# Kernel optimization log

Measured on AMD Instinct MI355X. Metric: run time of the kernel, lower is better.

Reference implementation:

```python
import jax, jax.numpy as jnp
import numpy as np

B, N_I, N_H1, N_H2, N_H3, N_H4 = 4096, 1024, 1024, 1024, 2048, 1024


def _linear_params(key, n_out, n_in, gain=1.0):
    kw, kb = jax.random.split(key)
    # xavier_uniform on weight, torch default uniform bias ~ U(-1/sqrt(n_in), 1/sqrt(n_in))
    limit = gain * np.sqrt(6.0 / (n_in + n_out))
    W = jax.random.uniform(kw, (n_out, n_in), jnp.float32, -limit, limit)
    bl = 1.0 / np.sqrt(n_in)
    b = jax.random.uniform(kb, (n_out,), jnp.float32, -bl, bl)
    return W, b


def setup_inputs() -> dict:
    key = jax.random.key(0)
    ks = jax.random.split(key, 16)
    inp = {
        "X": jax.random.normal(ks[0], (B, N_I), jnp.float32),
        "hidden1": jax.random.normal(ks[1], (B, N_H1), jnp.float32),
        "hidden2": jax.random.normal(ks[2], (B, N_H2), jnp.float32),
        "cell1": jax.random.normal(ks[3], (B, N_H1), jnp.float32),
        "cell2": jax.random.normal(ks[4], (B, N_H2), jnp.float32),
    }
    # LSTM1 gates: Linear(n_i + n_h1, n_h1)
    inp["Wf1"], inp["bf1"] = _linear_params(ks[5], N_H1, N_I + N_H1, 1.0)
    inp["Wi1"], inp["bi1"] = _linear_params(ks[6], N_H1, N_I + N_H1, 1.0)
    inp["Wc1"], inp["bc1"] = _linear_params(ks[7], N_H1, N_I + N_H1, 5.0 / 3.0)
    inp["Wo1"], inp["bo1"] = _linear_params(ks[8], N_H1, N_I + N_H1, 1.0)
    # LSTM2 gates: Linear(n_h1 + n_h2, n_h2)
    inp["Wf2"], inp["bf2"] = _linear_params(ks[9], N_H2, N_H1 + N_H2, 1.0)
    inp["Wi2"], inp["bi2"] = _linear_params(ks[10], N_H2, N_H1 + N_H2, 1.0)
    inp["Wc2"], inp["bc2"] = _linear_params(ks[11], N_H2, N_H1 + N_H2, 5.0 / 3.0)
    inp["Wo2"], inp["bo2"] = _linear_params(ks[12], N_H2, N_H1 + N_H2, 1.0)
    # MLP head
    inp["W3"], inp["b3"] = _linear_params(ks[13], N_H3, N_H2, np.sqrt(2.0))
    inp["W4"], inp["b4"] = _linear_params(ks[14], N_H4, N_H3, 1.0)
    return inp


def _lstm_cell(x, h, c, Wf, bf, Wi, bi, Wc, bc, Wo, bo):
    z = jnp.concatenate([x, h], axis=1)           # [B, n_i + n_h]
    f = jax.nn.sigmoid(z @ Wf.T + bf)
    i = jax.nn.sigmoid(z @ Wi.T + bi)
    cand = jnp.tanh(z @ Wc.T + bc)
    o = jax.nn.sigmoid(z @ Wo.T + bo)
    h_new = o * jnp.tanh(cand)                    # NOTE: double tanh, faithful to source
    c_new = f * c + cand * i
    return h_new, c_new


def reference(X, hidden1, hidden2, cell1, cell2,
              Wf1, bf1, Wi1, bi1, Wc1, bc1, Wo1, bo1,
              Wf2, bf2, Wi2, bi2, Wc2, bc2, Wo2, bo2,
              W3, b3, W4, b4):
    h1, c1 = _lstm_cell(X, hidden1, cell1, Wf1, bf1, Wi1, bi1, Wc1, bc1, Wo1, bo1)
    h2, c2 = _lstm_cell(h1, hidden2, cell2, Wf2, bf2, Wi2, bi2, Wc2, bc2, Wo2, bo2)
    out3 = jax.nn.relu(h2 @ W3.T + b3)
    out = out3 @ W4.T + b4
    return (out, h1, h2, c1, c2)
```

## Files before the change

### kernel.cpp

```cpp
#include <hip/hip_runtime.h>
#include <hip/hip_bf16.h>
#include <stdint.h>

typedef unsigned short u16;
typedef __bf16 bf16x8 __attribute__((ext_vector_type(8)));
typedef float f32x4 __attribute__((ext_vector_type(4)));
typedef float f32x8 __attribute__((ext_vector_type(8)));

#define BM 128
#define BN 128
#define BK 64

struct SegArgs {
  const u16* W[4];
  const float* b[4];
  void* out[4];
  int act[4];
  int bf16out[4];
};

__device__ __forceinline__ float bf2f(u16 u) {
  union { unsigned int i; float f; } v; v.i = ((unsigned int)u) << 16; return v.f;
}
__device__ __forceinline__ u16 f2bf(float f) {
  union { float f; unsigned int i; } v; v.f = f;
  return (u16)((v.i + 0x7fffu + ((v.i >> 16) & 1u)) >> 16);
}
__device__ __forceinline__ uint4 cvt8(f32x8 v) {
  uint4 r;
  r.x = (unsigned)f2bf(v[0]) | ((unsigned)f2bf(v[1]) << 16);
  r.y = (unsigned)f2bf(v[2]) | ((unsigned)f2bf(v[3]) << 16);
  r.z = (unsigned)f2bf(v[4]) | ((unsigned)f2bf(v[5]) << 16);
  r.w = (unsigned)f2bf(v[6]) | ((unsigned)f2bf(v[7]) << 16);
  return r;
}
__device__ __forceinline__ float actf(float x, int act) {
  if (act == 1) return 1.0f / (1.0f + __expf(-x));
  if (act == 2) {
    float xc = fminf(fmaxf(x, -15.0f), 15.0f);
    float e = __expf(2.0f * xc);
    return (e - 1.0f) / (e + 1.0f);
  }
  if (act == 3) return fmaxf(x, 0.0f);
  return x;
}

struct CvtArgs { const float* src[10]; u16* dst[10]; };
__global__ void cvt_f2b(CvtArgs a) {
  const float* s = a.src[blockIdx.y];
  u16* d = a.dst[blockIdx.y];
  int i0 = (blockIdx.x * 256 + threadIdx.x) * 8;
  f32x8 v = *(const f32x8*)(s + i0);
  *(uint4*)(d + i0) = cvt8(v);
}

__global__ __launch_bounds__(256, 2) void gemm_bt(
    const u16* __restrict__ A0, const u16* __restrict__ A1, int KA0, int K,
    SegArgs segs, int tileShift, int ldOut)
{
  __shared__ u16 As[BM * BK];
  __shared__ u16 Bs[BN * BK];

  const int tid  = threadIdx.x;
  const int lane = tid & 63;
  const int wave = tid >> 6;
  const int mBlock = blockIdx.x * BM;
  const int seg   = blockIdx.y >> tileShift;
  const int nTile = blockIdx.y & ((1 << tileShift) - 1);

  const u16* Wp = segs.W[seg];
  const int wm = wave & 1, wn = wave >> 1;

  const f32x4 zero = {0.f, 0.f, 0.f, 0.f};
  f32x4 acc[4][4];
#pragma unroll
  for (int i = 0; i < 4; ++i)
#pragma unroll
    for (int j = 0; j < 4; ++j) acc[i][j] = zero;

  for (int kb = 0; kb < K; kb += BK) {
    const u16* Aseg; int ka; int ldA;
    if (kb < KA0) { Aseg = A0; ka = kb;       ldA = KA0; }
    else          { Aseg = A1; ka = kb - KA0; ldA = K - KA0; }

#pragma unroll
    for (int it = 0; it < 4; ++it) {
      int s = it * 256 + tid;
      int m = s >> 3;
      int p = s & 7;
      int kc = p ^ (m & 7);
      const u16* srcA = Aseg + (size_t)(mBlock + m) * (size_t)ldA + (ka + kc * 8);
      const u16* srcB = Wp + (size_t)(nTile * BN + m) * (size_t)K + (kb + kc * 8);
      u16* dA = &As[(it * 256 + wave * 64) * 8];
      u16* dB = &Bs[(it * 256 + wave * 64) * 8];
      __builtin_amdgcn_global_load_lds((void*)srcA, (void*)dA, 16, 0, 0);
      __builtin_amdgcn_global_load_lds((void*)srcB, (void*)dB, 16, 0, 0);
    }
    __syncthreads();

#pragma unroll
    for (int ko = 0; ko < 2; ++ko) {
      bf16x8 af[4], bfr[4];
      int kcb = ko * 4 + (lane >> 4);
      int p = kcb ^ (lane & 7);
#pragma unroll
      for (int t = 0; t < 4; ++t) {
        int ml = wm * 64 + t * 16 + (lane & 15);
        af[t]  = *(const bf16x8*)&As[(ml * 8 + p) * 8];
        int nl = wn * 64 + t * 16 + (lane & 15);
        bfr[t] = *(const bf16x8*)&Bs[(nl * 8 + p) * 8];
      }
#pragma unroll
      for (int tm = 0; tm < 4; ++tm)
#pragma unroll
        for (int tn = 0; tn < 4; ++tn)
          acc[tm][tn] = __builtin_amdgcn_mfma_f32_16x16x32_bf16(af[tm], bfr[tn], acc[tm][tn], 0, 0, 0);
    }
    __syncthreads();
  }

  const float* bp = segs.b[seg];
  const int act = segs.act[seg];
  const int isBf = segs.bf16out[seg];
  u16*   opb = (u16*)segs.out[seg];
  float* opf = (float*)segs.out[seg];
  const int q  = lane >> 4;
  const int cl = lane & 15;
#pragma unroll
  for (int tn = 0; tn < 4; ++tn) {
    int col = nTile * BN + wn * 64 + tn * 16 + cl;
    float bv = bp[col];
#pragma unroll
    for (int tm = 0; tm < 4; ++tm) {
      int row = mBlock + wm * 64 + tm * 16 + q * 4;
#pragma unroll
      for (int r = 0; r < 4; ++r) {
        float v = actf(acc[tm][tn][r] + bv, act);
        size_t idx = (size_t)(row + r) * (size_t)ldOut + col;
        if (isBf) opb[idx] = f2bf(v); else opf[idx] = v;
      }
    }
  }
}

__global__ void lstm_ew(const u16* __restrict__ gates, const float* __restrict__ cold,
                        float* __restrict__ hout, float* __restrict__ cout,
                        u16* __restrict__ hb, int n)
{
  int i0 = (blockIdx.x * blockDim.x + threadIdx.x) * 8;
  if (i0 >= n) return;
  union U { uint4 v; u16 u[8]; };
  U F, I, C, O;
  F.v = *(const uint4*)(gates + i0);
  I.v = *(const uint4*)(gates + (size_t)n + i0);
  C.v = *(const uint4*)(gates + 2 * (size_t)n + i0);
  O.v = *(const uint4*)(gates + 3 * (size_t)n + i0);
  f32x8 c0v = *(const f32x8*)(cold + i0);
  f32x8 H, CN;
#pragma unroll
  for (int j = 0; j < 8; ++j) {
    float f  = bf2f(F.u[j]);
    float ig = bf2f(I.u[j]);
    float cd = bf2f(C.u[j]);
    float o  = bf2f(O.u[j]);
    float cn = f * c0v[j] + cd * ig;
    float e  = __expf(2.0f * cd);
    float th = (e - 1.0f) / (e + 1.0f);
    H[j]  = o * th;
    CN[j] = cn;
  }
  *(f32x8*)(hout + i0) = H;
  *(f32x8*)(cout + i0) = CN;
  *(uint4*)(hb + i0) = cvt8(H);
}

extern "C" void kernel_launch(void* const* d_in, const int* in_sizes, int n_in,
                              void* d_out, int out_size, void* d_ws, size_t ws_size,
                              hipStream_t stream)
{
  const size_t P   = 4096ull * 1024ull;
  const size_t C2M = 2097152ull;

  const float* X   = (const float*)d_in[0];
  const float* h1i = (const float*)d_in[1];
  const float* h2i = (const float*)d_in[2];
  const float* c1i = (const float*)d_in[3];
  const float* c2i = (const float*)d_in[4];
  const float* Wf1 = (const float*)d_in[5];  const float* bf1_ = (const float*)d_in[6];
  const float* Wi1 = (const float*)d_in[7];  const float* bi1_ = (const float*)d_in[8];
  const float* Wc1 = (const float*)d_in[9];  const float* bc1_ = (const float*)d_in[10];
  const float* Wo1 = (const float*)d_in[11]; const float* bo1_ = (const float*)d_in[12];
  const float* Wf2 = (const float*)d_in[13]; const float* bf2_ = (const float*)d_in[14];
  const float* Wi2 = (const float*)d_in[15]; const float* bi2_ = (const float*)d_in[16];
  const float* Wc2 = (const float*)d_in[17]; const float* bc2_ = (const float*)d_in[18];
  const float* Wo2 = (const float*)d_in[19]; const float* bo2_ = (const float*)d_in[20];
  const float* W3  = (const float*)d_in[21]; const float* b3_  = (const float*)d_in[22];
  const float* W4  = (const float*)d_in[23]; const float* b4_  = (const float*)d_in[24];

  float* out = (float*)d_out;
  float* h1  = out + P;
  float* h2  = out + 2 * P;
  float* c1  = out + 3 * P;
  float* c2  = out + 4 * P;

  char* ws = (char*)d_ws;
  u16* gates = (u16*)ws;
  u16* Areg  = (u16*)(ws + (32ull << 20));
  u16* Breg  = (u16*)(ws + (48ull << 20));
  u16* Creg  = (u16*)(ws + (56ull << 20));
  u16* Ereg  = (u16*)(ws + (64ull << 20));
  u16* Freg  = (u16*)(ws + (72ull << 20));

  dim3 blk(256, 1, 1);

  CvtArgs ca;
  ca.src[0]=Wf1;        ca.dst[0]=Areg;
  ca.src[1]=Wi1;        ca.dst[1]=Areg + C2M;
  ca.src[2]=Wc1;        ca.dst[2]=Areg + 2*C2M;
  ca.src[3]=Wo1;        ca.dst[3]=Areg + 3*C2M;
  ca.src[4]=X;          ca.dst[4]=Breg;
  ca.src[5]=X + C2M;    ca.dst[5]=Breg + C2M;
  ca.src[6]=h1i;        ca.dst[6]=Creg;
  ca.src[7]=h1i + C2M;  ca.dst[7]=Creg + C2M;
  ca.src[8]=W3;         ca.dst[8]=Freg;
  ca.src[9]=W4;         ca.dst[9]=Freg + C2M;
  cvt_f2b<<<dim3(1024, 10, 1), blk, 0, stream>>>(ca);

  SegArgs s1;
  s1.W[0]=Areg; s1.W[1]=Areg+C2M; s1.W[2]=Areg+2*C2M; s1.W[3]=Areg+3*C2M;
  s1.b[0]=bf1_; s1.b[1]=bi1_; s1.b[2]=bc1_; s1.b[3]=bo1_;
  s1.out[0]=gates; s1.out[1]=gates+P; s1.out[2]=gates+2*P; s1.out[3]=gates+3*P;
  s1.act[0]=1; s1.act[1]=1; s1.act[2]=2; s1.act[3]=1;
  s1.bf16out[0]=s1.bf16out[1]=s1.bf16out[2]=s1.bf16out[3]=1;
  gemm_bt<<<dim3(32,32,1), blk, 0, stream>>>(Breg, Creg, 1024, 2048, s1, 3, 1024);
  lstm_ew<<<dim3(2048,1,1), blk, 0, stream>>>(gates, c1i, h1, c1, Ereg, (int)P);

  CvtArgs cb;
  cb.src[0]=Wf2;        cb.dst[0]=Areg;
  cb.src[1]=Wi2;        cb.dst[1]=Areg + C2M;
  cb.src[2]=Wc2;        cb.dst[2]=Areg + 2*C2M;
  cb.src[3]=Wo2;        cb.dst[3]=Areg + 3*C2M;
  cb.src[4]=h2i;        cb.dst[4]=Breg;
  cb.src[5]=h2i + C2M;  cb.dst[5]=Breg + C2M;
  cvt_f2b<<<dim3(1024, 6, 1), blk, 0, stream>>>(cb);

  SegArgs s2 = s1;
  s2.b[0]=bf2_; s2.b[1]=bi2_; s2.b[2]=bc2_; s2.b[3]=bo2_;
  gemm_bt<<<dim3(32,32,1), blk, 0, stream>>>(Ereg, Breg, 1024, 2048, s2, 3, 1024);
  lstm_ew<<<dim3(2048,1,1), blk, 0, stream>>>(gates, c2i, h2, c2, Creg, (int)P);

  SegArgs s3;
  for (int g = 0; g < 4; ++g) { s3.W[g]=Freg; s3.b[g]=b3_; s3.out[g]=Areg; s3.act[g]=3; s3.bf16out[g]=1; }
  gemm_bt<<<dim3(32,16,1), blk, 0, stream>>>(Creg, (const u16*)nullptr, 1024, 1024, s3, 4, 2048);

  SegArgs s4;
  for (int g = 0; g < 4; ++g) { s4.W[g]=Freg+C2M; s4.b[g]=b4_; s4.out[g]=out; s4.act[g]=0; s4.bf16out[g]=0; }
  gemm_bt<<<dim3(32,8,1), blk, 0, stream>>>(Areg, (const u16*)nullptr, 2048, 2048, s4, 3, 1024);
}
```

Before: 490.5 us.

## Add 256x256-tile GEMM with 4-stage async LDS pipeline for LSTM gate GEMMs

Adds a new GEMM kernel for the two LSTM gate GEMMs. It uses 512 threads, 256x256 output tiles and BK=32, and streams tiles from global memory straight into LDS through global_load_lds with a 4-deep ring buffer and XOR swizzle. Larger tiles raise operand reuse and the asynchronous multi-stage pipeline overlaps loads with MFMA. In exchange the kernel uses 128KB of LDS and many accumulator registers, and the grid shrinks to 256 blocks, which may hurt occupancy or leave CUs idle.

Result: no change. 499.4 us (+1.8%).

```diff
diff --git a/kernel.cpp b/kernel.cpp
--- a/kernel.cpp
+++ b/kernel.cpp
@@ -52,6 +52,114 @@
   int i0 = (blockIdx.x * 256 + threadIdx.x) * 8;
   f32x8 v = *(const f32x8*)(s + i0);
   *(uint4*)(d + i0) = cvt8(v);
+}
+
+#define G2M 256
+#define G2K 32
+
+__global__ __launch_bounds__(512, 2) void gemm_bt2(
+    const u16* __restrict__ A0, const u16* __restrict__ A1, int KA0, int K,
+    SegArgs segs, int tileShift, int ldOut)
+{
+  __shared__ u16 smem[4 * 16384];
+
+  const int tid  = threadIdx.x;
+  const int lane = tid & 63;
+  const int wave = tid >> 6;
+  const int wm = wave & 1, wn = wave >> 1;
+  const int mBlock  = blockIdx.x * G2M;
+  const int seg     = blockIdx.y >> tileShift;
+  const int nTile   = blockIdx.y & ((1 << tileShift) - 1);
+  const int colBase = nTile * G2M;
+  const u16* Wp = segs.W[seg];
+  const int NT = K / G2K;
+
+  auto STAGE = [&](int kt) {
+    int kb = kt * G2K;
+    const u16* Aseg; int ka, ldA;
+    if (kb < KA0) { Aseg = A0; ka = kb;       ldA = KA0; }
+    else          { Aseg = A1; ka = kb - KA0; ldA = K - KA0; }
+    u16* base = &smem[(kt & 3) * 16384];
+#pragma unroll
+    for (int it = 0; it < 2; ++it) {
+      int g   = it * 512 + tid;
+      int row = g >> 2;
+      int c   = (g & 3) ^ ((row >> 1) & 3);
+      const u16* srcA = Aseg + (size_t)(mBlock  + row) * (size_t)ldA + (ka + c * 8);
+      const u16* srcB = Wp   + (size_t)(colBase + row) * (size_t)K   + (kb + c * 8);
+      u16* dA = base +        (it * 512 + wave * 64) * 8;
+      u16* dB = base + 8192 + (it * 512 + wave * 64) * 8;
+      __builtin_amdgcn_global_load_lds((void*)srcA, (void*)dA, 16, 0, 0);
+      __builtin_amdgcn_global_load_lds((void*)srcB, (void*)dB, 16, 0, 0);
+    }
+  };
+
+  const f32x4 zero = {0.f, 0.f, 0.f, 0.f};
+  f32x4 acc[8][4];
+#pragma unroll
+  for (int m = 0; m < 8; ++m)
+#pragma unroll
+    for (int n = 0; n < 4; ++n) acc[m][n] = zero;
+
+  STAGE(0); STAGE(1); STAGE(2);
+
+  for (int t = 0; t < NT; ++t) {
+    if      (t + 3 <= NT) asm volatile("s_waitcnt vmcnt(8)" ::: "memory");
+    else if (t + 2 <= NT) asm volatile("s_waitcnt vmcnt(4)" ::: "memory");
+    else                  asm volatile("s_waitcnt vmcnt(0)" ::: "memory");
+    __builtin_amdgcn_sched_barrier(0);
+    __builtin_amdgcn_s_barrier();
+    __builtin_amdgcn_sched_barrier(0);
+
+    if (t + 3 < NT) STAGE(t + 3);
+
+    const u16* Ab = &smem[(t & 3) * 16384];
+    const u16* Bb = Ab + 8192;
+    const int q = lane >> 4;
+    bf16x8 af[8], bfr[4];
+#pragma unroll
+    for (int m = 0; m < 8; ++m) {
+      int r = wm * 128 + m * 16 + (lane & 15);
+      int p = q ^ ((r >> 1) & 3);
+      af[m] = *(const bf16x8*)(Ab + (r * 4 + p) * 8);
+    }
+#pragma unroll
+    for (int n = 0; n < 4; ++n) {
+      int r = wn * 64 + n * 16 + (lane & 15);
+      int p = q ^ ((r >> 1) & 3);
+      bfr[n] = *(const bf16x8*)(Bb + (r * 4 + p) * 8);
+    }
+    __builtin_amdgcn_s_setprio(1);
+#pragma unroll
+    for (int m = 0; m < 8; ++m)
+#pragma unroll
+      for (int n = 0; n < 4; ++n)
+        acc[m][n] = __builtin_amdgcn_mfma_f32_16x16x32_bf16(af[m], bfr[n], acc[m][n], 0, 0, 0);
+    __builtin_amdgcn_s_setprio(0);
+  }
+
+  const float* bp = segs.b[seg];
+  const int act  = segs.act[seg];
+  const int isBf = segs.bf16out[seg];
+  u16*   opb = (u16*)segs.out[seg];
+  float* opf = (float*)segs.out[seg];
+  const int q4 = (lane >> 4) * 4;
+  const int cl = lane & 15;
+#pragma unroll
+  for (int n = 0; n < 4; ++n) {
+    int col = colBase + wn * 64 + n * 16 + cl;
+    float bv = bp[col];
+#pragma unroll
+    for (int m = 0; m < 8; ++m) {
+      int row = mBlock + wm * 128 + m * 16 + q4;
+#pragma unroll
+      for (int r = 0; r < 4; ++r) {
+        float v = actf(acc[m][n][r] + bv, act);
+        size_t idx = (size_t)(row + r) * (size_t)ldOut + col;
+        if (isBf) opb[idx] = f2bf(v); else opf[idx] = v;
+      }
+    }
+  }
 }
 
 __global__ __launch_bounds__(256, 2) void gemm_bt(
@@ -212,6 +320,7 @@
   u16* Freg  = (u16*)(ws + (72ull << 20));
 
   dim3 blk(256, 1, 1);
+  dim3 blk2(512, 1, 1);
 
   CvtArgs ca;
   ca.src[0]=Wf1;        ca.dst[0]=Areg;
@@ -232,7 +341,7 @@
   s1.out[0]=gates; s1.out[1]=gates+P; s1.out[2]=gates+2*P; s1.out[3]=gates+3*P;
   s1.act[0]=1; s1.act[1]=1; s1.act[2]=2; s1.act[3]=1;
   s1.bf16out[0]=s1.bf16out[1]=s1.bf16out[2]=s1.bf16out[3]=1;
-  gemm_bt<<<dim3(32,32,1), blk, 0, stream>>>(Breg, Creg, 1024, 2048, s1, 3, 1024);
+  gemm_bt2<<<dim3(16,16,1), blk2, 0, stream>>>(Breg, Creg, 1024, 2048, s1, 2, 1024);
   lstm_ew<<<dim3(2048,1,1), blk, 0, stream>>>(gates, c1i, h1, c1, Ereg, (int)P);
 
   CvtArgs cb;
@@ -246,7 +355,7 @@
 
   SegArgs s2 = s1;
   s2.b[0]=bf2_; s2.b[1]=bi2_; s2.b[2]=bc2_; s2.b[3]=bo2_;
-  gemm_bt<<<dim3(32,32,1), blk, 0, stream>>>(Ereg, Breg, 1024, 2048, s2, 3, 1024);
+  gemm_bt2<<<dim3(16,16,1), blk2, 0, stream>>>(Ereg, Breg, 1024, 2048, s2, 2, 1024);
   lstm_ew<<<dim3(2048,1,1), blk, 0, stream>>>(gates, c2i, h2, c2, Creg, (int)P);
 
   SegArgs s3;
```

## Fuse LSTM elementwise update into gate GEMM epilogue with interleaved gate columns

Applied to the files above, without the earlier changes.

Adds a gemm_lstm kernel whose B tile interleaves the four gate weight rows, so each group of four adjacent output columns holds f,i,c,o for one hidden unit. The epilogue applies the gate activations, exchanges them across lanes with shuffles, and computes h and c directly. The separate lstm_ew kernel and the bf16 gates buffer round-trip are removed for both LSTM layers. In exchange, epilogue stores and cold-state loads become narrow and scattered, and extra shuffles and divergent activation math are added.

Result: slower. 538.6 us (+9.8%).

```diff
diff --git a/kernel.cpp b/kernel.cpp
--- a/kernel.cpp
+++ b/kernel.cpp
@@ -19,6 +19,15 @@
   int bf16out[4];
 };
 
+struct LstmArgs {
+  const u16* W[4];
+  const float* b[4];
+  const float* cold;
+  float* h;
+  float* c;
+  u16*   hb;
+};
+
 __device__ __forceinline__ float bf2f(u16 u) {
   union { unsigned int i; float f; } v; v.i = ((unsigned int)u) << 16; return v.f;
 }
@@ -52,6 +61,125 @@
   int i0 = (blockIdx.x * 256 + threadIdx.x) * 8;
   f32x8 v = *(const f32x8*)(s + i0);
   *(uint4*)(d + i0) = cvt8(v);
+}
+
+__global__ __launch_bounds__(256, 2) void gemm_lstm(
+    const u16* __restrict__ A0, const u16* __restrict__ A1, int KA0, int K,
+    LstmArgs La)
+{
+  __shared__ u16 As[BM * BK];
+  __shared__ u16 Bs[BN * BK];
+
+  const int tid  = threadIdx.x;
+  const int lane = tid & 63;
+  const int wave = tid >> 6;
+  const int mBlock = blockIdx.x * BM;
+  const int nTile  = blockIdx.y;
+  const int wm = wave & 1, wn = wave >> 1;
+
+  const u16* pA[4];
+  const u16* pB[4];
+#pragma unroll
+  for (int it = 0; it < 4; ++it) {
+    int s  = it * 256 + tid;
+    int m  = s >> 3;
+    int kc = (s & 7) ^ (m & 7);
+    int gate = m & 3;
+    int realcol = nTile * 32 + (m >> 2);
+    const u16* w = (gate == 0) ? La.W[0] : (gate == 1) ? La.W[1]
+                 : (gate == 2) ? La.W[2] : La.W[3];
+    pB[it] = w + (size_t)realcol * (size_t)K + kc * 8;
+    pA[it] = A0 + (size_t)(mBlock + m) * (size_t)KA0 + kc * 8;
+  }
+
+  const f32x4 zero = {0.f, 0.f, 0.f, 0.f};
+  f32x4 acc[4][4];
+#pragma unroll
+  for (int i = 0; i < 4; ++i)
+#pragma unroll
+    for (int j = 0; j < 4; ++j) acc[i][j] = zero;
+
+  for (int kb = 0; kb < K; kb += BK) {
+    if (kb == KA0) {
+#pragma unroll
+      for (int it = 0; it < 4; ++it) {
+        int s  = it * 256 + tid;
+        int m  = s >> 3;
+        int kc = (s & 7) ^ (m & 7);
+        pA[it] = A1 + (size_t)(mBlock + m) * (size_t)(K - KA0) + kc * 8;
+      }
+    }
+#pragma unroll
+    for (int it = 0; it < 4; ++it) {
+      u16* dA = &As[(it * 256 + wave * 64) * 8];
+      u16* dB = &Bs[(it * 256 + wave * 64) * 8];
+      __builtin_amdgcn_global_load_lds((void*)pA[it], (void*)dA, 16, 0, 0);
+      __builtin_amdgcn_global_load_lds((void*)pB[it], (void*)dB, 16, 0, 0);
+      pA[it] += BK; pB[it] += BK;
+    }
+    __syncthreads();
+
+#pragma unroll
+    for (int ko = 0; ko < 2; ++ko) {
+      bf16x8 af[4], bfr[4];
+      int kcb = ko * 4 + (lane >> 4);
+      int p = kcb ^ (lane & 7);
+#pragma unroll
+      for (int t = 0; t < 4; ++t) {
+        int ml = wm * 64 + t * 16 + (lane & 15);
+        af[t]  = *(const bf16x8*)&As[(ml * 8 + p) * 8];
+        int nl = wn * 64 + t * 16 + (lane & 15);
+        bfr[t] = *(const bf16x8*)&Bs[(nl * 8 + p) * 8];
+      }
+#pragma unroll
+      for (int tm = 0; tm < 4; ++tm)
+#pragma unroll
+        for (int tn = 0; tn < 4; ++tn)
+          acc[tm][tn] = __builtin_amdgcn_mfma_f32_16x16x32_bf16(af[tm], bfr[tn], acc[tm][tn], 0, 0, 0);
+    }
+    __syncthreads();
+  }
+
+  const int g  = lane & 3;
+  const int cl = lane & 15;
+  const int q4 = (lane >> 4) * 4;
+  const bool isT = (g == 2);
+  const float* bsel = (g == 0) ? La.b[0] : (g == 1) ? La.b[1]
+                    : (g == 2) ? La.b[2] : La.b[3];
+  const bool g1 = (g & 1) != 0, g2v = (g & 2) != 0;
+#pragma unroll
+  for (int tn = 0; tn < 4; ++tn) {
+    int col = nTile * 32 + wn * 16 + tn * 4 + (cl >> 2);
+    float bv = bsel[col];
+#pragma unroll
+    for (int tm = 0; tm < 4; ++tm) {
+      int rowbase = mBlock + wm * 64 + tm * 16 + q4;
+#pragma unroll
+      for (int r = 0; r < 4; ++r) {
+        float x  = acc[tm][tn][r] + bv;
+        float xc = isT ? fminf(fmaxf(x, -15.f), 15.f) : x;
+        float e  = __expf(isT ? 2.f * xc : -x);
+        float a  = isT ? (e - 1.f) / (e + 1.f) : 1.f / (1.f + e);
+        float x1 = __shfl_xor(a, 1);
+        float x2 = __shfl_xor(a, 2);
+        float x3 = __shfl_xor(a, 3);
+        float fv = g1 ? (g2v ? x3 : x1) : (g2v ? x2 : a);
+        float iv = g1 ? (g2v ? x2 : a ) : (g2v ? x3 : x1);
+        float cd = g1 ? (g2v ? x1 : x3) : (g2v ? a  : x2);
+        float ov = g1 ? (g2v ? a  : x2) : (g2v ? x1 : x3);
+        if (g == r) {
+          size_t idx = (size_t)(rowbase + r) * 1024 + col;
+          float cn = fv * La.cold[idx] + cd * iv;
+          float e2 = __expf(2.f * cd);
+          float th = (e2 - 1.f) / (e2 + 1.f);
+          float hv = ov * th;
+          La.h[idx]  = hv;
+          La.c[idx]  = cn;
+          La.hb[idx] = f2bf(hv);
+        }
+      }
+    }
+  }
 }
 
 __global__ __launch_bounds__(256, 2) void gemm_bt(
@@ -141,37 +269,6 @@
       }
     }
   }
-}
-
-__global__ void lstm_ew(const u16* __restrict__ gates, const float* __restrict__ cold,
-                        float* __restrict__ hout, float* __restrict__ cout,
-                        u16* __restrict__ hb, int n)
-{
-  int i0 = (blockIdx.x * blockDim.x + threadIdx.x) * 8;
-  if (i0 >= n) return;
-  union U { uint4 v; u16 u[8]; };
-  U F, I, C, O;
-  F.v = *(const uint4*)(gates + i0);
-  I.v = *(const uint4*)(gates + (size_t)n + i0);
-  C.v = *(const uint4*)(gates + 2 * (size_t)n + i0);
-  O.v = *(const uint4*)(gates + 3 * (size_t)n + i0);
-  f32x8 c0v = *(const f32x8*)(cold + i0);
-  f32x8 H, CN;
-#pragma unroll
-  for (int j = 0; j < 8; ++j) {
-    float f  = bf2f(F.u[j]);
-    float ig = bf2f(I.u[j]);
-    float cd = bf2f(C.u[j]);
-    float o  = bf2f(O.u[j]);
-    float cn = f * c0v[j] + cd * ig;
-    float e  = __expf(2.0f * cd);
-    float th = (e - 1.0f) / (e + 1.0f);
-    H[j]  = o * th;
-    CN[j] = cn;
-  }
-  *(f32x8*)(hout + i0) = H;
-  *(f32x8*)(cout + i0) = CN;
-  *(uint4*)(hb + i0) = cvt8(H);
 }
 
 extern "C" void kernel_launch(void* const* d_in, const int* in_sizes, int n_in,
@@ -204,7 +301,6 @@
   float* c2  = out + 4 * P;
 
   char* ws = (char*)d_ws;
-  u16* gates = (u16*)ws;
   u16* Areg  = (u16*)(ws + (32ull << 20));
   u16* Breg  = (u16*)(ws + (48ull << 20));
   u16* Creg  = (u16*)(ws + (56ull << 20));
@@ -226,14 +322,11 @@
   ca.src[9]=W4;         ca.dst[9]=Freg + C2M;
   cvt_f2b<<<dim3(1024, 10, 1), blk, 0, stream>>>(ca);
 
-  SegArgs s1;
-  s1.W[0]=Areg; s1.W[1]=Areg+C2M; s1.W[2]=Areg+2*C2M; s1.W[3]=Areg+3*C2M;
-  s1.b[0]=bf1_; s1.b[1]=bi1_; s1.b[2]=bc1_; s1.b[3]=bo1_;
-  s1.out[0]=gates; s1.out[1]=gates+P; s1.out[2]=gates+2*P; s1.out[3]=gates+3*P;
-  s1.act[0]=1; s1.act[1]=1; s1.act[2]=2; s1.act[3]=1;
-  s1.bf16out[0]=s1.bf16out[1]=s1.bf16out[2]=s1.bf16out[3]=1;
-  gemm_bt<<<dim3(32,32,1), blk, 0, stream>>>(Breg, Creg, 1024, 2048, s1, 3, 1024);
-  lstm_ew<<<dim3(2048,1,1), blk, 0, stream>>>(gates, c1i, h1, c1, Ereg, (int)P);
+  LstmArgs l1;
+  l1.W[0]=Areg; l1.W[1]=Areg+C2M; l1.W[2]=Areg+2*C2M; l1.W[3]=Areg+3*C2M;
+  l1.b[0]=bf1_; l1.b[1]=bi1_; l1.b[2]=bc1_; l1.b[3]=bo1_;
+  l1.cold=c1i; l1.h=h1; l1.c=c1; l1.hb=Ereg;
+  gemm_lstm<<<dim3(32,32,1), blk, 0, stream>>>(Breg, Creg, 1024, 2048, l1);
 
   CvtArgs cb;
   cb.src[0]=Wf2;        cb.dst[0]=Areg;
@@ -244,10 +337,11 @@
   cb.src[5]=h2i + C2M;  cb.dst[5]=Breg + C2M;
   cvt_f2b<<<dim3(1024, 6, 1), blk, 0, stream>>>(cb);
 
-  SegArgs s2 = s1;
-  s2.b[0]=bf2_; s2.b[1]=bi2_; s2.b[2]=bc2_; s2.b[3]=bo2_;
-  gemm_bt<<<dim3(32,32,1), blk, 0, stream>>>(Ereg, Breg, 1024, 2048, s2, 3, 1024);
-  lstm_ew<<<dim3(2048,1,1), blk, 0, stream>>>(gates, c2i, h2, c2, Creg, (int)P);
+  LstmArgs l2;
+  l2.W[0]=Areg; l2.W[1]=Areg+C2M; l2.W[2]=Areg+2*C2M; l2.W[3]=Areg+3*C2M;
+  l2.b[0]=bf2_; l2.b[1]=bi2_; l2.b[2]=bc2_; l2.b[3]=bo2_;
+  l2.cold=c2i; l2.h=h2; l2.c=c2; l2.hb=Creg;
+  gemm_lstm<<<dim3(32,32,1), blk, 0, stream>>>(Ereg, Breg, 1024, 2048, l2);
 
   SegArgs s3;
   for (int g = 0; g < 4; ++g) { s3.W[g]=Freg; s3.b[g]=b3_; s3.out[g]=Areg; s3.act[g]=3; s3.bf16out[g]=1; }
```
